# Performance work log

Hardware: AMD Instinct MI355X
Metric: run time of the kernel (lower is better)

The kernel has to match this reference:

```python
import jax, jax.numpy as jnp
import numpy as np

D_MODEL = 1024
N_HEAD = 16
D_HEAD = D_MODEL // N_HEAD
SEQ = 1024
RLEN = 2 * SEQ
BATCH = 4
LN_EPS = 1e-5


def setup_inputs() -> dict:
    key = jax.random.key(0)
    ks = jax.random.split(key, 12)
    s = 0.02
    return {
        "h": jax.random.normal(ks[0], (SEQ, BATCH, D_MODEL), jnp.float32),
        "r": jax.random.normal(ks[1], (RLEN, BATCH, D_MODEL), jnp.float32),
        "q_w": jax.random.normal(ks[2], (D_MODEL, N_HEAD, D_HEAD), jnp.float32) * s,
        "k_w": jax.random.normal(ks[3], (D_MODEL, N_HEAD, D_HEAD), jnp.float32) * s,
        "v_w": jax.random.normal(ks[4], (D_MODEL, N_HEAD, D_HEAD), jnp.float32) * s,
        "o_w": jax.random.normal(ks[5], (D_MODEL, N_HEAD, D_HEAD), jnp.float32) * s,
        "r_w": jax.random.normal(ks[6], (D_MODEL, N_HEAD, D_HEAD), jnp.float32) * s,
        "r_r_bias": jax.random.normal(ks[7], (N_HEAD, D_HEAD), jnp.float32) * s,
        "r_w_bias": jax.random.normal(ks[8], (N_HEAD, D_HEAD), jnp.float32) * s,
        "ln_gamma": jnp.ones((D_MODEL,), jnp.float32),
        "ln_beta": jnp.zeros((D_MODEL,), jnp.float32),
    }


def rel_shift_bnij(x, klen):
    # x: [b, n, i, j]; Transformer-XL relative-shift trick
    b, n, i, j = x.shape
    x = x.reshape(b, n, j, i)[:, :, 1:, :].reshape(b, n, i, j - 1)
    return x[:, :, :, :klen]


def reference(h, r, q_w, k_w, v_w, o_w, r_w, r_r_bias, r_w_bias, ln_gamma, ln_beta):
    scale = 1.0 / np.sqrt(D_HEAD).astype(np.float32)
    # projections: i=seq, b=batch, n=heads, d=head dim
    q_head = jnp.einsum('ibh,hnd->ibnd', h, q_w)
    k_head = jnp.einsum('ibh,hnd->ibnd', h, k_w)
    v_head = jnp.einsum('ibh,hnd->ibnd', h, v_w)
    k_head_r = jnp.einsum('ibh,hnd->ibnd', r, r_w)
    # content and position attention scores
    ac = jnp.einsum('ibnd,jbnd->bnij', q_head + r_w_bias, k_head)
    bd = jnp.einsum('ibnd,jbnd->bnij', q_head + r_r_bias, k_head_r)
    bd = rel_shift_bnij(bd, klen=ac.shape[3])
    attn_prob = jax.nn.softmax((ac + bd) * scale, axis=3)  # dropout is identity at eval
    attn_vec = jnp.einsum('bnij,jbnd->ibnd', attn_prob, v_head)
    attn_out = jnp.einsum('ibnd,hnd->ibh', attn_vec, o_w) + h  # residual
    mu = jnp.mean(attn_out, axis=-1, keepdims=True)
    var = jnp.var(attn_out, axis=-1, keepdims=True)
    return (attn_out - mu) / jnp.sqrt(var + LN_EPS) * ln_gamma + ln_beta
```

## Files before the change

kernel.cpp:

```cpp
#include <hip/hip_runtime.h>
#include <stdint.h>


typedef __attribute__((ext_vector_type(8))) short v8s;
typedef __attribute__((ext_vector_type(4))) float v4f;

__device__ __forceinline__ uint16_t f2b(float x) {
    uint32_t u = __builtin_bit_cast(uint32_t, x);
    u += 0x7fffu + ((u >> 16) & 1u);
    return (uint16_t)(u >> 16);
}

__device__ __forceinline__ void gld16(const void* g, void* lds) {
    __builtin_amdgcn_global_load_lds(
        (const __attribute__((address_space(1))) uint32_t*)g,
        (__attribute__((address_space(3))) uint32_t*)lds, 16, 0, 0);
}

__global__ __launch_bounds__(256) void prep_kernel(
    const float* __restrict__ h, const float* __restrict__ r,
    const float* __restrict__ o_w, const float* __restrict__ q_w,
    const float* __restrict__ k_w, const float* __restrict__ v_w,
    const float* __restrict__ r_w,
    uint64_t* __restrict__ hB, uint64_t* __restrict__ rB,
    uint64_t* __restrict__ owB, uint16_t* __restrict__ Wcat,
    uint16_t* __restrict__ rwT)
{
    __shared__ float t[64][65];
    const int bid = blockIdx.x, tid = threadIdx.x;
    if (bid < 1024) {
        const int tx = bid & 15, ty = (bid >> 4) & 15, z = bid >> 8;
        const int n0 = tx * 64, h0 = ty * 64;
        const float* src = (z == 0) ? q_w : (z == 1) ? k_w : (z == 2) ? v_w : r_w;
        uint16_t* dst = (z == 3) ? rwT : Wcat + (size_t)z * 1048576;
#pragma unroll
        for (int q = 0; q < 16; ++q) {
            int idx = q * 256 + tid, rr = idx >> 6, cc = idx & 63;
            t[rr][cc] = src[(size_t)(h0 + rr) * 1024 + n0 + cc];
        }
        __syncthreads();
#pragma unroll
        for (int q = 0; q < 16; ++q) {
            int idx = q * 256 + tid, rr = idx >> 6, cc = idx & 63;
            dst[(size_t)(n0 + rr) * 1024 + h0 + cc] = f2b(t[cc][rr]);
        }
    } else {
        const float4* h4 = (const float4*)h;
        const float4* r4 = (const float4*)r;
        const float4* w4 = (const float4*)o_w;
        const int total = 1048576 + 2097152 + 262144;
        for (int i = (bid - 1024) * 256 + tid; i < total; i += 2048 * 256) {
            float4 v; uint64_t* dst; int idx;
            if (i < 1048576)      { idx = i;           v = h4[idx]; dst = hB; }
            else if (i < 3145728) { idx = i - 1048576; v = r4[idx]; dst = rB; }
            else                  { idx = i - 3145728; v = w4[idx]; dst = owB; }
            uint64_t p = (uint64_t)f2b(v.x) | ((uint64_t)f2b(v.y) << 16)
                       | ((uint64_t)f2b(v.z) << 32) | ((uint64_t)f2b(v.w) << 48);
            dst[idx] = p;
        }
    }
}

template<int MODE, int MI>
__device__ __forceinline__ void gemm_body(
    const uint16_t* __restrict__ A, const uint16_t* __restrict__ B, int K,
    int bx, int by, uint16_t* As, uint16_t* Bs,
    uint16_t* __restrict__ o0, uint16_t* __restrict__ o1,
    uint16_t* __restrict__ o2, uint16_t* __restrict__ o3,
    const float* __restrict__ bias0, const float* __restrict__ bias1,
    float* __restrict__ fo, const float* __restrict__ fres)
{
    const int tid = threadIdx.x;
    const int w = tid >> 6, lane = tid & 63;
    const int g = lane >> 4, c15 = lane & 15;
    const int m0 = by * (MI * 32), n0 = bx * 128;
    const int wr = w >> 1, wc = w & 1;

    int rowA[MI], colA[MI];
#pragma unroll
    for (int q = 0; q < MI; ++q) {
        int D = (w * MI + q) * 1024 + lane * 16;
        int row = D >> 7;
        rowA[q] = row;
        colA[q] = (D & 127) ^ ((row & 7) << 4);
    }
    int rowB[4], colB[4];
#pragma unroll
    for (int q = 0; q < 4; ++q) {
        int D = (w * 4 + q) * 1024 + lane * 16;
        int row = D >> 7;
        rowB[q] = row;
        colB[q] = (D & 127) ^ ((row & 7) << 4);
    }

    v4f acc[MI][4];
#pragma unroll
    for (int i = 0; i < MI; ++i)
#pragma unroll
        for (int j = 0; j < 4; ++j) acc[i][j] = v4f{0.f, 0.f, 0.f, 0.f};

    const char* Abase = (const char*)(A + (size_t)m0 * K);
    const char* Bbase = (const char*)(B + (size_t)n0 * K);
    const size_t ld = (size_t)K * 2;

    for (int kb = 0; kb < K; kb += 64) {
        if (kb) __syncthreads();
#pragma unroll
        for (int q = 0; q < MI; ++q)
            gld16(Abase + (size_t)rowA[q] * ld + (size_t)kb * 2 + colA[q],
                  (char*)As + (w * MI + q) * 1024);
#pragma unroll
        for (int q = 0; q < 4; ++q)
            gld16(Bbase + (size_t)rowB[q] * ld + (size_t)kb * 2 + colB[q],
                  (char*)Bs + (w * 4 + q) * 1024);
        asm volatile("s_waitcnt vmcnt(0)" ::: "memory");
        __syncthreads();

        v8s af[MI][2], bf[4][2];
#pragma unroll
        for (int mi = 0; mi < MI; ++mi) {
            int row = wr * (MI * 16) + mi * 16 + c15;
#pragma unroll
            for (int ks = 0; ks < 2; ++ks) {
                int cl = ks * 64 + g * 16;
                af[mi][ks] = *(const v8s*)((const char*)As + row * 128 + (cl ^ ((row & 7) << 4)));
            }
        }
#pragma unroll
        for (int ni = 0; ni < 4; ++ni) {
            int row = wc * 64 + ni * 16 + c15;
#pragma unroll
            for (int ks = 0; ks < 2; ++ks) {
                int cl = ks * 64 + g * 16;
                bf[ni][ks] = *(const v8s*)((const char*)Bs + row * 128 + (cl ^ ((row & 7) << 4)));
            }
        }
#pragma unroll
        for (int mi = 0; mi < MI; ++mi)
#pragma unroll
            for (int ni = 0; ni < 4; ++ni)
#pragma unroll
                for (int ks = 0; ks < 2; ++ks)
                    acc[mi][ni] = __builtin_amdgcn_mfma_f32_16x16x32_bf16(
                        af[mi][ks], bf[ni][ks], acc[mi][ni], 0, 0, 0);
    }

#pragma unroll
    for (int mi = 0; mi < MI; ++mi)
#pragma unroll
        for (int ni = 0; ni < 4; ++ni)
#pragma unroll
            for (int t = 0; t < 4; ++t) {
                int row = m0 + wr * (MI * 16) + mi * 16 + g * 4 + t;
                int col = n0 + wc * 64 + ni * 16 + c15;
                float v = acc[mi][ni][t];
                if (MODE == 0) {
                    int seg = col >> 10, nd = col & 1023;
                    int i = row >> 2, b = row & 3, n = nd >> 6, d = nd & 63;
                    int bn = b * 16 + n;
                    if (seg == 0) {
                        o0[(bn << 16) + (i << 6) + d] = f2b(v + bias0[nd]);
                        o1[(bn << 16) + (i << 6) + d] = f2b(v + bias1[nd]);
                    } else if (seg == 1) {
                        o2[(bn << 16) + (i << 6) + d] = f2b(v);
                    } else {
                        int il = i & 63;
                        int iperm = (i & ~63) | ((il & 15) * 4 + (il >> 4));
                        o3[(bn << 16) + (d << 10) + iperm] = f2b(v);
                    }
                } else if (MODE == 1) {
                    int j = row >> 2, b = row & 3, n = col >> 6, d = col & 63;
                    int bn = b * 16 + n;
                    o0[(bn << 17) + (j << 6) + d] = f2b(v);
                } else {
                    size_t idx = (size_t)row * 1024 + col;
                    fo[idx] = v + fres[idx];
                }
            }
}

__global__ __launch_bounds__(256) void gemm_qkvr(
    const uint16_t* __restrict__ hB, const uint16_t* __restrict__ Wcat,
    const uint16_t* __restrict__ rB, const uint16_t* __restrict__ rwT,
    uint16_t* __restrict__ Qw, uint16_t* __restrict__ Qr,
    uint16_t* __restrict__ Kt, uint16_t* __restrict__ Vt,
    uint16_t* __restrict__ Kr,
    const float* __restrict__ b0, const float* __restrict__ b1)
{
    __shared__ __align__(16) uint16_t As[128 * 64];
    __shared__ __align__(16) uint16_t Bs[128 * 64];
    const int bid = blockIdx.x;
    if (bid < 768) {
        gemm_body<0, 4>(hB, Wcat, 1024, bid % 24, bid / 24, As, Bs,
                        Qw, Qr, Kt, Vt, b0, b1, nullptr, nullptr);
    } else {
        const int b2 = bid - 768;
        gemm_body<1, 4>(rB, rwT, 1024, b2 % 8, b2 / 8, As, Bs,
                        Kr, nullptr, nullptr, nullptr, nullptr, nullptr,
                        nullptr, nullptr);
    }
}

__global__ __launch_bounds__(256) void gemm_out(
    const uint16_t* __restrict__ AV, const uint16_t* __restrict__ owB,
    float* __restrict__ AO, const float* __restrict__ hres)
{
    __shared__ __align__(16) uint16_t As[64 * 64];
    __shared__ __align__(16) uint16_t Bs[128 * 64];
    gemm_body<2, 2>(AV, owB, 1024, blockIdx.x % 8, blockIdx.x / 8, As, Bs,
                    nullptr, nullptr, nullptr, nullptr, nullptr, nullptr,
                    AO, hres);
}

__global__ __launch_bounds__(512, 4) void attn_kernel(
    const uint16_t* __restrict__ Qw, const uint16_t* __restrict__ Qr,
    const uint16_t* __restrict__ Kt, const uint16_t* __restrict__ Vt,
    const uint16_t* __restrict__ Kr, uint16_t* __restrict__ AV)
{
    __shared__ __align__(16) uint16_t Ks[2][4096];
    __shared__ __align__(16) uint16_t Vs[2][4096];
    __shared__ __align__(16) uint16_t Krs[16384];
    __shared__ __align__(16) uint16_t Ptl[8][1024];

    const int tid = threadIdx.x, w = tid >> 6, lane = tid & 63;
    const int g = lane >> 4, c15 = lane & 15;
    const int bid = blockIdx.x;
    const int xcd = bid & 7, slot = bid >> 3;
    const int it = slot & 7, bn = ((slot >> 3) << 3) | xcd;
    const int b = bn >> 4, n = bn & 15;
    const int i0 = it * 128, i0w = i0 + w * 16;
    const int B0 = 897 - i0;

    const uint16_t* qwp = Qw + ((size_t)bn << 16);
    const uint16_t* qrp = Qr + ((size_t)bn << 16);
    const char* ktp = (const char*)(Kt + ((size_t)bn << 16));
    const char* vtp = (const char*)(Vt + ((size_t)bn << 16));
    const char* krp = (const char*)(Kr + ((size_t)bn << 17));

    const int rsub = lane >> 3;
    const int csrc = ((lane & 7) ^ rsub) << 4;
    const int dsto = lane * 16;
    const int swz = (c15 & 7) << 4;

    int sl[4], esel[4];
#pragma unroll
    for (int t = 0; t < 4; ++t) {
        int e = 15 + c15 - (g * 4 + t);
        sl[t] = g * 16 + (e & 15);
        esel[t] = e >> 4;
    }

    v8s qwf[2], qrf[2];
#pragma unroll
    for (int ks = 0; ks < 2; ++ks) {
        qwf[ks] = *(const v8s*)(qwp + ((i0w + c15) << 6) + ks * 32 + g * 8);
        qrf[ks] = *(const v8s*)(qrp + ((i0w + c15) << 6) + ks * 32 + g * 8);
    }

    v4f acc_o[4];
    float psac[4];
#pragma unroll
    for (int df = 0; df < 4; ++df) acc_o[df] = v4f{0.f, 0.f, 0.f, 0.f};
#pragma unroll
    for (int t = 0; t < 4; ++t) psac[t] = 0.f;

    uint16_t* Ptw = Ptl[w];
    const float SCL = 0.18033688f;
    const float MB8 = 11.54156032f;

    gld16(ktp + (size_t)(w * 8 + rsub) * 128 + csrc,
          (char*)Ks[0] + w * 1024 + dsto);
    gld16(vtp + (size_t)(w * 8 + rsub) * 2048 + csrc,
          (char*)Vs[0] + w * 1024 + dsto);
#pragma unroll
    for (int qq = 0; qq < 3; ++qq) {
        const int chunk = qq * 8 + w;
        const int rg = B0 + chunk * 8 + rsub;
        gld16(krp + (size_t)rg * 128 + csrc, (char*)Krs + chunk * 1024 + dsto);
    }
    asm volatile("s_waitcnt vmcnt(0)" ::: "memory");
    __syncthreads();

    for (int jt = 0; jt < 16; ++jt) {
        const int cur = jt & 1;
        if (jt < 15) {
            const int j1 = (jt + 1) * 64;
            gld16(ktp + (size_t)(j1 + w * 8 + rsub) * 128 + csrc,
                  (char*)Ks[cur ^ 1] + w * 1024 + dsto);
            gld16(vtp + (size_t)(w * 8 + rsub) * 2048 + j1 * 2 + csrc,
                  (char*)Vs[cur ^ 1] + w * 1024 + dsto);
            const int sbase = (192 + 64 * jt) & 255;
            int rg = B0 + 192 + 64 * jt + w * 8 + rsub;
            rg = rg > 2047 ? 2047 : rg;
            gld16(krp + (size_t)rg * 128 + csrc,
                  (char*)Krs + (sbase + w * 8) * 128 + dsto);
        }

        v4f ac[4];
#pragma unroll
        for (int jf = 0; jf < 4; ++jf) ac[jf] = v4f{0.f, 0.f, 0.f, 0.f};
        v4f pp[5];
#pragma unroll
        for (int pf = 0; pf < 5; ++pf) pp[pf] = v4f{0.f, 0.f, 0.f, 0.f};

        __builtin_amdgcn_s_setprio(1);
#pragma unroll
        for (int jf = 0; jf < 4; ++jf) {
            const char* krow = (const char*)Ks[cur] + (jf * 16 + c15) * 128;
#pragma unroll
            for (int ks = 0; ks < 2; ++ks) {
                v8s kf = *(const v8s*)(krow + ((ks * 64 + g * 16) ^ swz));
                ac[jf] = __builtin_amdgcn_mfma_f32_16x16x32_bf16(qwf[ks], kf, ac[jf], 0, 0, 0);
            }
        }
        const int krbase = 64 * jt + 112 - 16 * w + c15;
#pragma unroll
        for (int pf = 0; pf < 5; ++pf) {
            const int sltr = (krbase + 16 * pf) & 255;
            const char* krow = (const char*)Krs + sltr * 128;
#pragma unroll
            for (int ks = 0; ks < 2; ++ks) {
                v8s krf = *(const v8s*)(krow + ((ks * 64 + g * 16) ^ swz));
                pp[pf] = __builtin_amdgcn_mfma_f32_16x16x32_bf16(qrf[ks], krf, pp[pf], 0, 0, 0);
            }
        }
        __builtin_amdgcn_s_setprio(0);

        float spp[5][4];
#pragma unroll
        for (int pf = 0; pf < 5; ++pf)
#pragma unroll
            for (int t = 0; t < 4; ++t)
                spp[pf][t] = __shfl(pp[pf][t], sl[t]);

#pragma unroll
        for (int t = 0; t < 4; ++t) {
            float p[4];
#pragma unroll
            for (int jf = 0; jf < 4; ++jf) {
                float bd = esel[t] ? spp[jf + 1][t] : spp[jf][t];
                p[jf] = exp2f((ac[jf][t] + bd) * SCL - MB8);
                psac[t] += p[jf];
            }
            uint32_t w0 = (uint32_t)f2b(p[0]) | ((uint32_t)f2b(p[1]) << 16);
            uint32_t w1 = (uint32_t)f2b(p[2]) | ((uint32_t)f2b(p[3]) << 16);
            const int rw = g * 4 + t;
            *(uint2*)((char*)Ptw + rw * 128 + ((c15 * 8) ^ ((rw & 7) << 4))) =
                uint2{w0, w1};
        }
        asm volatile("s_waitcnt lgkmcnt(0)" ::: "memory");

        v8s pa[2];
#pragma unroll
        for (int ks = 0; ks < 2; ++ks)
            pa[ks] = *(const v8s*)((const char*)Ptw + c15 * 128 + ((ks * 64 + g * 16) ^ swz));
        __builtin_amdgcn_s_setprio(1);
#pragma unroll
        for (int df = 0; df < 4; ++df) {
            const char* vrow = (const char*)Vs[cur] + (df * 16 + c15) * 128;
#pragma unroll
            for (int ks = 0; ks < 2; ++ks) {
                v8s vf = *(const v8s*)(vrow + ((ks * 64 + g * 16) ^ swz));
                acc_o[df] = __builtin_amdgcn_mfma_f32_16x16x32_bf16(pa[ks], vf, acc_o[df], 0, 0, 0);
            }
        }
        __builtin_amdgcn_s_setprio(0);

        asm volatile("s_waitcnt vmcnt(0)" ::: "memory");
        __syncthreads();
    }

    float rinv[4];
#pragma unroll
    for (int t = 0; t < 4; ++t) {
        float l = psac[t];
#pragma unroll
        for (int m = 1; m < 16; m <<= 1) l += __shfl_xor(l, m);
        rinv[t] = 1.0f / l;
    }
#pragma unroll
    for (int df = 0; df < 4; ++df)
#pragma unroll
        for (int t = 0; t < 4; ++t) {
            int i = i0w + g * 4 + t;
            int d = df * 16 + c15;
            AV[((size_t)(i * 4 + b) << 10) + n * 64 + d] =
                f2b(acc_o[df][t] * rinv[t]);
        }
}

__global__ __launch_bounds__(256) void ln_kernel(
    const float* __restrict__ AO, const float* __restrict__ gamma,
    const float* __restrict__ beta, float* __restrict__ out)
{
    const int w = threadIdx.x >> 6, lane = threadIdx.x & 63;
    const int row = blockIdx.x * 4 + w;
    const float4* src = (const float4*)(AO + (size_t)row * 1024);
    float4 v[4];
    float s = 0.f, sq = 0.f;
#pragma unroll
    for (int q = 0; q < 4; ++q) {
        v[q] = src[lane + q * 64];
        s += v[q].x + v[q].y + v[q].z + v[q].w;
        sq += v[q].x * v[q].x + v[q].y * v[q].y + v[q].z * v[q].z + v[q].w * v[q].w;
    }
#pragma unroll
    for (int m = 1; m < 64; m <<= 1) { s += __shfl_xor(s, m); sq += __shfl_xor(sq, m); }
    float mean = s * (1.f / 1024.f);
    float var = sq * (1.f / 1024.f) - mean * mean;
    float rstd = rsqrtf(var + 1e-5f);
    const float4* g4 = (const float4*)gamma;
    const float4* b4 = (const float4*)beta;
    float4* o4 = (float4*)(out + (size_t)row * 1024);
#pragma unroll
    for (int q = 0; q < 4; ++q) {
        float4 gg = g4[lane + q * 64], bb = b4[lane + q * 64], vv = v[q], r;
        r.x = (vv.x - mean) * rstd * gg.x + bb.x;
        r.y = (vv.y - mean) * rstd * gg.y + bb.y;
        r.z = (vv.z - mean) * rstd * gg.z + bb.z;
        r.w = (vv.w - mean) * rstd * gg.w + bb.w;
        o4[lane + q * 64] = r;
    }
}

extern "C" void kernel_launch(void* const* d_in, const int* in_sizes, int n_in,
                              void* d_out, int out_size, void* d_ws, size_t ws_size,
                              hipStream_t stream)
{
    const float* h        = (const float*)d_in[0];
    const float* r        = (const float*)d_in[1];
    const float* q_w      = (const float*)d_in[2];
    const float* k_w      = (const float*)d_in[3];
    const float* v_w      = (const float*)d_in[4];
    const float* o_w      = (const float*)d_in[5];
    const float* r_w      = (const float*)d_in[6];
    const float* r_r_bias = (const float*)d_in[7];
    const float* r_w_bias = (const float*)d_in[8];
    const float* ln_gamma = (const float*)d_in[9];
    const float* ln_beta  = (const float*)d_in[10];
    float* out = (float*)d_out;

    char* ws = (char*)d_ws;
    const size_t MB = 1u << 20;
    uint16_t* hB   = (uint16_t*)(ws + 0);
    uint16_t* rB   = (uint16_t*)(ws + 8 * MB);
    uint16_t* Wcat = (uint16_t*)(ws + 24 * MB);
    uint16_t* rwT  = (uint16_t*)(ws + 30 * MB);
    uint16_t* owB  = (uint16_t*)(ws + 32 * MB);
    uint16_t* Qw   = (uint16_t*)(ws + 34 * MB);
    uint16_t* Qr   = (uint16_t*)(ws + 42 * MB);
    uint16_t* Kt   = (uint16_t*)(ws + 50 * MB);
    uint16_t* Vt   = (uint16_t*)(ws + 58 * MB);
    uint16_t* Kr   = (uint16_t*)(ws + 66 * MB);
    uint16_t* AV   = hB;
    float*    AO   = (float*)rB;

    prep_kernel<<<3072, 256, 0, stream>>>(h, r, o_w, q_w, k_w, v_w, r_w,
                                          (uint64_t*)hB, (uint64_t*)rB,
                                          (uint64_t*)owB, Wcat, rwT);
    gemm_qkvr<<<1280, 256, 0, stream>>>(hB, Wcat, rB, rwT,
                                        Qw, Qr, Kt, Vt, Kr, r_w_bias, r_r_bias);
    attn_kernel<<<512, 512, 0, stream>>>(Qw, Qr, Kt, Vt, Kr, AV);
    gemm_out<<<512, 256, 0, stream>>>(AV, owB, AO, h);
    ln_kernel<<<1024, 256, 0, stream>>>(AO, ln_gamma, ln_beta, out);
}
```

Before: 160.4 us.

## Double-buffer GEMM LDS tiles, remap blocks per XCD, use packed bf16 convert

The GEMM main loop now double-buffers its LDS tiles, issuing the async global-to-LDS loads for the next K-slab before the MFMAs on the current one. This hides load latency and removes one barrier per iteration, at the cost of twice the LDS per block, which can lower occupancy. Block indices in the projection and output GEMMs are remapped so that blocks sharing an XCD work on neighbouring tiles, which should improve L2 reuse. In the attention kernel, the software bf16 rounding of the probabilities is replaced by the hardware v_cvt_pk_bf16_f32 instruction.

Result: no change. 161.6 us (+0.7%).

```diff
diff --git a/kernel.cpp b/kernel.cpp
--- a/kernel.cpp
+++ b/kernel.cpp
@@ -75,6 +75,8 @@
     const int g = lane >> 4, c15 = lane & 15;
     const int m0 = by * (MI * 32), n0 = bx * 128;
     const int wr = w >> 1, wc = w & 1;
+    const int ABUF = MI * 2048;
+    const int BBUF = 8192;
 
     int rowA[MI], colA[MI];
 #pragma unroll
@@ -103,19 +105,27 @@
     const char* Bbase = (const char*)(B + (size_t)n0 * K);
     const size_t ld = (size_t)K * 2;
 
-    for (int kb = 0; kb < K; kb += 64) {
-        if (kb) __syncthreads();
+    auto stage = [&](int buf, int kb) {
 #pragma unroll
         for (int q = 0; q < MI; ++q)
             gld16(Abase + (size_t)rowA[q] * ld + (size_t)kb * 2 + colA[q],
-                  (char*)As + (w * MI + q) * 1024);
+                  (char*)(As + buf * ABUF) + (w * MI + q) * 1024);
 #pragma unroll
         for (int q = 0; q < 4; ++q)
             gld16(Bbase + (size_t)rowB[q] * ld + (size_t)kb * 2 + colB[q],
-                  (char*)Bs + (w * 4 + q) * 1024);
-        asm volatile("s_waitcnt vmcnt(0)" ::: "memory");
-        __syncthreads();
-
+                  (char*)(Bs + buf * BBUF) + (w * 4 + q) * 1024);
+    };
+
+    stage(0, 0);
+    asm volatile("s_waitcnt vmcnt(0)" ::: "memory");
+    __syncthreads();
+
+    int buf = 0;
+    for (int kb = 0; kb < K; kb += 64) {
+        if (kb + 64 < K) stage(buf ^ 1, kb + 64);
+
+        const char* Ab = (const char*)(As + buf * ABUF);
+        const char* Bb = (const char*)(Bs + buf * BBUF);
         v8s af[MI][2], bf[4][2];
 #pragma unroll
         for (int mi = 0; mi < MI; ++mi) {
@@ -123,7 +133,7 @@
 #pragma unroll
             for (int ks = 0; ks < 2; ++ks) {
                 int cl = ks * 64 + g * 16;
-                af[mi][ks] = *(const v8s*)((const char*)As + row * 128 + (cl ^ ((row & 7) << 4)));
+                af[mi][ks] = *(const v8s*)(Ab + row * 128 + (cl ^ ((row & 7) << 4)));
             }
         }
 #pragma unroll
@@ -132,7 +142,7 @@
 #pragma unroll
             for (int ks = 0; ks < 2; ++ks) {
                 int cl = ks * 64 + g * 16;
-                bf[ni][ks] = *(const v8s*)((const char*)Bs + row * 128 + (cl ^ ((row & 7) << 4)));
+                bf[ni][ks] = *(const v8s*)(Bb + row * 128 + (cl ^ ((row & 7) << 4)));
             }
         }
 #pragma unroll
@@ -143,6 +153,10 @@
                 for (int ks = 0; ks < 2; ++ks)
                     acc[mi][ni] = __builtin_amdgcn_mfma_f32_16x16x32_bf16(
                         af[mi][ks], bf[ni][ks], acc[mi][ni], 0, 0, 0);
+
+        asm volatile("s_waitcnt vmcnt(0)" ::: "memory");
+        __syncthreads();
+        buf ^= 1;
     }
 
 #pragma unroll
@@ -187,15 +201,21 @@
     uint16_t* __restrict__ Kr,
     const float* __restrict__ b0, const float* __restrict__ b1)
 {
-    __shared__ __align__(16) uint16_t As[128 * 64];
-    __shared__ __align__(16) uint16_t Bs[128 * 64];
+    __shared__ __align__(16) uint16_t As[2 * 128 * 64];
+    __shared__ __align__(16) uint16_t Bs[2 * 128 * 64];
     const int bid = blockIdx.x;
     if (bid < 768) {
-        gemm_body<0, 4>(hB, Wcat, 1024, bid % 24, bid / 24, As, Bs,
+        const int x = bid & 7, l = bid >> 3;
+        const int by = (x >> 1) * 8 + l / 12;
+        const int bx = (x & 1) * 12 + l % 12;
+        gemm_body<0, 4>(hB, Wcat, 1024, bx, by, As, Bs,
                         Qw, Qr, Kt, Vt, b0, b1, nullptr, nullptr);
     } else {
         const int b2 = bid - 768;
-        gemm_body<1, 4>(rB, rwT, 1024, b2 % 8, b2 / 8, As, Bs,
+        const int x = b2 & 7, l = b2 >> 3;
+        const int by = x * 8 + l / 8;
+        const int bx = l % 8;
+        gemm_body<1, 4>(rB, rwT, 1024, bx, by, As, Bs,
                         Kr, nullptr, nullptr, nullptr, nullptr, nullptr,
                         nullptr, nullptr);
     }
@@ -205,9 +225,12 @@
     const uint16_t* __restrict__ AV, const uint16_t* __restrict__ owB,
     float* __restrict__ AO, const float* __restrict__ hres)
 {
-    __shared__ __align__(16) uint16_t As[64 * 64];
-    __shared__ __align__(16) uint16_t Bs[128 * 64];
-    gemm_body<2, 2>(AV, owB, 1024, blockIdx.x % 8, blockIdx.x / 8, As, Bs,
+    __shared__ __align__(16) uint16_t As[2 * 64 * 64];
+    __shared__ __align__(16) uint16_t Bs[2 * 128 * 64];
+    const int x = blockIdx.x & 7, l = blockIdx.x >> 3;
+    const int by = x * 8 + l / 8;
+    const int bx = l % 8;
+    gemm_body<2, 2>(AV, owB, 1024, bx, by, As, Bs,
                     nullptr, nullptr, nullptr, nullptr, nullptr, nullptr,
                     AO, hres);
 }
@@ -342,8 +365,9 @@
                 p[jf] = exp2f((ac[jf][t] + bd) * SCL - MB8);
                 psac[t] += p[jf];
             }
-            uint32_t w0 = (uint32_t)f2b(p[0]) | ((uint32_t)f2b(p[1]) << 16);
-            uint32_t w1 = (uint32_t)f2b(p[2]) | ((uint32_t)f2b(p[3]) << 16);
+            uint32_t w0, w1;
+            asm("v_cvt_pk_bf16_f32 %0, %1, %2" : "=v"(w0) : "v"(p[0]), "v"(p[1]));
+            asm("v_cvt_pk_bf16_f32 %0, %1, %2" : "=v"(w1) : "v"(p[2]), "v"(p[3]));
             const int rw = g * 4 + t;
             *(uint2*)((char*)Ptw + rw * 128 + ((c15 * 8) ^ ((rw & 7) << 4))) =
                 uint2{w0, w1};
```
